# Performance work log

Hardware: AMD Instinct MI355X
Metric: run time of the kernel (lower is better)

## Reference

```python
import jax, jax.numpy as jnp
import numpy as np

B, T = 128, 512
V, P, K = 10002, 500, 20
DC, DP, DT = 300, 100, 50
D = DC + DP + DT
H = 256


def setup_inputs() -> dict:
    key = jax.random.key(0)
    ks = jax.random.split(key, 21)
    s = lambda i, shape: jax.random.normal(ks[i], shape, jnp.float32) * 0.05
    return dict(
        x=jax.random.randint(ks[0], (B, T), 0, V),
        y=jax.random.randint(ks[1], (B, T), 0, K),
        pre_tags=jax.random.randint(ks[2], (B, T), 0, K),
        pinyin_tags=jax.random.randint(ks[3], (B, T), 0, P),
        mask=jnp.ones((B, T), bool),
        char_emb=s(4, (V, DC)),
        tag_emb=s(5, (K, DT)),
        pinyin_emb=s(6, (P, DP)),
        w_ih_f=s(7, (4 * H, D)), w_hh_f=s(8, (4 * H, H)), b_ih_f=s(9, (4 * H,)), b_hh_f=s(10, (4 * H,)),
        w_ih_b=s(11, (4 * H, D)), w_hh_b=s(12, (4 * H, H)), b_ih_b=s(13, (4 * H,)), b_hh_b=s(14, (4 * H,)),
        w_out=s(15, (K, 2 * H)), b_out=s(16, (K,)),
        start_trans=s(17, (K,)), end_trans=s(18, (K,)), trans=s(19, (K, K)),
    )


def _lstm_dir(xs, w_ih, w_hh, b_ih, b_hh, reverse):
    # xs: [T,B,D]; precompute input projection for all steps (one big GEMM)
    pre = jnp.einsum('tbd,gd->tbg', xs, w_ih) + b_ih + b_hh  # [T,B,4H]
    bsz = xs.shape[1]

    def step(carry, gx):
        h, c = carry
        g = gx + h @ w_hh.T
        i, f, gg, o = jnp.split(g, 4, axis=-1)  # torch gate order i,f,g,o
        c = jax.nn.sigmoid(f) * c + jax.nn.sigmoid(i) * jnp.tanh(gg)
        h = jax.nn.sigmoid(o) * jnp.tanh(c)
        return (h, c), h

    init = (jnp.zeros((bsz, H), xs.dtype), jnp.zeros((bsz, H), xs.dtype))
    _, hs = jax.lax.scan(step, init, pre, reverse=reverse)
    return hs  # [T,B,H]


def _emissions(x, pre_tags, pinyin_tags, char_emb, tag_emb, pinyin_emb,
               w_ih_f, w_hh_f, b_ih_f, b_hh_f, w_ih_b, w_hh_b, b_ih_b, b_hh_b,
               w_out, b_out):
    emb = jnp.concatenate([char_emb[x], pinyin_emb[pinyin_tags], tag_emb[pre_tags]], axis=2)  # [B,T,D]
    xs = emb.transpose(1, 0, 2)  # [T,B,D]
    hf = _lstm_dir(xs, w_ih_f, w_hh_f, b_ih_f, b_hh_f, reverse=False)
    hb = _lstm_dir(xs, w_ih_b, w_hh_b, b_ih_b, b_hh_b, reverse=True)
    h = jnp.concatenate([hf, hb], axis=-1)  # [T,B,2H]
    return jnp.einsum('tbh,kh->tbk', h, w_out) + b_out  # emissions [T,B,K]


def _crf_nll(em, tags, mask, start, trans, end):
    # em [T,B,K] (time-major), torchcrf forward with reduction='sum'
    tg = tags.T  # [T,B]
    mk = mask.T.astype(em.dtype)  # [T,B]
    # gold-path score
    first = start[tg[0]] + jnp.take_along_axis(em[0], tg[0][:, None], 1)[:, 0]

    def num_step(score, inputs):
        e_t, t_prev, t_cur, m = inputs
        s = trans[t_prev, t_cur] + jnp.take_along_axis(e_t, t_cur[:, None], 1)[:, 0]
        return score + s * m, None

    score, _ = jax.lax.scan(num_step, first, (em[1:], tg[:-1], tg[1:], mk[1:]))
    last_idx = (mask.sum(1) - 1).astype(jnp.int32)
    last_tag = jnp.take_along_axis(tags, last_idx[:, None].astype(tags.dtype), 1)[:, 0]
    score = score + end[last_tag]
    # partition function via forward algorithm
    alpha0 = start[None, :] + em[0]  # [B,K]

    def den_step(alpha, inputs):
        e_t, m = inputs
        nxt = jax.nn.logsumexp(alpha[:, :, None] + trans[None, :, :] + e_t[:, None, :], axis=1)
        return jnp.where(m[:, None] > 0, nxt, alpha), None

    alpha, _ = jax.lax.scan(den_step, alpha0, (em[1:], mk[1:]))
    logZ = jax.nn.logsumexp(alpha + end[None, :], axis=1)
    llh = jnp.sum(score - logZ)
    return -llh  # module returns -crf(...)


def reference(x, y, pre_tags, pinyin_tags, mask, char_emb, tag_emb, pinyin_emb,
              w_ih_f, w_hh_f, b_ih_f, b_hh_f, w_ih_b, w_hh_b, b_ih_b, b_hh_b,
              w_out, b_out, start_trans, end_trans, trans):
    em = _emissions(x, pre_tags, pinyin_tags, char_emb, tag_emb, pinyin_emb,
                    w_ih_f, w_hh_f, b_ih_f, b_hh_f, w_ih_b, w_hh_b, b_ih_b, b_hh_b,
                    w_out, b_out)
    return _crf_nll(em, y, mask, start_trans, trans, end_trans)
```

## Files before the change

kernel.cpp:

```cpp
#include <hip/hip_runtime.h>
#include <hip/hip_bf16.h>

typedef __attribute__((ext_vector_type(8))) short short8;
typedef __attribute__((ext_vector_type(4))) float float4v;
typedef __attribute__((ext_vector_type(4))) int int4v;

__device__ __forceinline__ float sigmoidf_(float x) {
  return __fdividef(1.f, 1.f + __expf(-x));
}
__device__ __forceinline__ float tanhf_(float x) {
  float e = __expf(2.f * x);
  return 1.f - __fdividef(2.f, e + 1.f);
}
__device__ __forceinline__ float bflo(unsigned int v) {
  return __uint_as_float(v << 16);
}
__device__ __forceinline__ float bfhi(unsigned int v) {
  return __uint_as_float(v & 0xffff0000u);
}
__device__ __forceinline__ void barrier_lgkm() {
  asm volatile("s_waitcnt lgkmcnt(0)\n\ts_barrier" ::: "memory");
}

__device__ __forceinline__ unsigned int pack4_(float4 v, float inv) {
  int b0 = (int)rintf(v.x * inv), b1 = (int)rintf(v.y * inv);
  int b2 = (int)rintf(v.z * inv), b3 = (int)rintf(v.w * inv);
  return (unsigned int)((b0 & 0xff) | ((b1 & 0xff) << 8) | ((b2 & 0xff) << 16) |
                        ((b3 & 0xff) << 24));
}

__device__ __forceinline__ int sel4_(int4v v, int rr) {
  int a = (rr & 1) ? v[1] : v[0];
  int b = (rr & 1) ? v[3] : v[2];
  return (rr & 2) ? b : a;
}

__global__ __launch_bounds__(256) void wquant_kernel(
    const float* __restrict__ whh_f, const float* __restrict__ whh_b,
    unsigned int* __restrict__ wq, float* __restrict__ wsc) {
  const int wave_g = blockIdx.x * 4 + (threadIdx.x >> 6);
  const int lane = threadIdx.x & 63;
  const int dir = wave_g >> 10, row = wave_g & 1023;
  const float* __restrict__ src = (dir ? whh_b : whh_f) + (size_t)row * 256;
  float4 v = ((const float4*)src)[lane];
  float mx = fmaxf(fmaxf(fabsf(v.x), fabsf(v.y)), fmaxf(fabsf(v.z), fabsf(v.w)));
#pragma unroll
  for (int k = 32; k >= 1; k >>= 1) mx = fmaxf(mx, __shfl_xor(mx, k, 64));
  float inv = (mx > 0.f) ? __fdividef(127.f, mx) : 0.f;
  wq[(size_t)wave_g * 64 + lane] = pack4_(v, inv);
  if (lane == 0) wsc[wave_g] = (mx > 0.f) ? (mx / (127.f * 127.f)) : 0.f;
}

__global__ __launch_bounds__(256) void proj_gemm(
    const float* __restrict__ A, int rowsA, int Kdim, int col_off,
    const float* __restrict__ wf, const float* __restrict__ wb,
    const float* __restrict__ bf1, const float* __restrict__ bf2,
    const float* __restrict__ bb1, const float* __restrict__ bb2,
    __hip_bfloat16* __restrict__ out, int add_bias) {
  __shared__ __align__(16) __hip_bfloat16 As[128][40];
  __shared__ __align__(16) __hip_bfloat16 Bs[256][40];
  const int tid = threadIdx.x;
  const int m0 = blockIdx.x * 128, n0 = blockIdx.y * 256;
  const int lane = tid & 63, wave = tid >> 6;
  const int quad = lane >> 4, lm = lane & 15;
  float4v acc[2][16] = {};
  const int ksteps = (Kdim + 31) >> 5;
  const int r2 = tid >> 1, cbase = (tid & 1) << 4;
  const int rb = tid >> 4, cb = (tid & 15) * 2;
  for (int ks = 0; ks < ksteps; ++ks) {
    const int k0 = ks << 5;
#pragma unroll
    for (int e2 = 0; e2 < 8; ++e2) {
      int kk = k0 + cbase + 2 * e2;
      float b0 = 0.f, b1 = 0.f;
      if (m0 + r2 < rowsA && kk < Kdim) {
        float2 v = *(const float2*)(A + (size_t)(m0 + r2) * Kdim + kk);
        b0 = v.x;
        b1 = v.y;
      }
      As[r2][cbase + 2 * e2] = __float2bfloat16(b0);
      As[r2][cbase + 2 * e2 + 1] = __float2bfloat16(b1);
    }
#pragma unroll
    for (int j = 0; j < 16; ++j) {
      int n = n0 + rb + 16 * j;
      const float* __restrict__ wrow =
          (n < 1024) ? (wf + n * 450 + col_off) : (wb + (n - 1024) * 450 + col_off);
      int kk = k0 + cb;
      float b0 = 0.f, b1 = 0.f;
      if (kk < Kdim) {
        float2 v = *(const float2*)(wrow + kk);
        b0 = v.x;
        b1 = v.y;
      }
      Bs[rb + 16 * j][cb] = __float2bfloat16(b0);
      Bs[rb + 16 * j][cb + 1] = __float2bfloat16(b1);
    }
    __syncthreads();
    short8 af0 = *(const short8*)(&As[wave * 32 + lm][quad * 8]);
    short8 af1 = *(const short8*)(&As[wave * 32 + 16 + lm][quad * 8]);
#pragma unroll
    for (int t = 0; t < 16; ++t) {
      short8 bf = *(const short8*)(&Bs[t * 16 + lm][quad * 8]);
      acc[0][t] = __builtin_amdgcn_mfma_f32_16x16x32_bf16(af0, bf, acc[0][t], 0, 0, 0);
      acc[1][t] = __builtin_amdgcn_mfma_f32_16x16x32_bf16(af1, bf, acc[1][t], 0, 0, 0);
    }
    __syncthreads();
  }
#pragma unroll
  for (int mg = 0; mg < 2; ++mg) {
#pragma unroll
    for (int t = 0; t < 16; ++t) {
#pragma unroll
      for (int rr = 0; rr < 4; ++rr) {
        int m = m0 + wave * 32 + mg * 16 + quad * 4 + rr;
        int col = n0 + t * 16 + lm;
        if (m < rowsA) {
          float v = acc[mg][t][rr];
          if (add_bias)
            v += (col < 1024) ? (bf1[col] + bf2[col]) : (bb1[col - 1024] + bb2[col - 1024]);
          int dir = col >> 10, rq = col & 1023;
          int gate = rq >> 8, u = rq & 255;
          out[m * 2048 + dir * 1024 + u * 4 + gate] = __float2bfloat16(v);
        }
      }
    }
  }
}

__global__ __launch_bounds__(512, 2) void lstm_kernel(
    const unsigned int* __restrict__ wq, const float* __restrict__ wsc,
    const int* __restrict__ x, const int* __restrict__ ptags, const int* __restrict__ gtags,
    const char* __restrict__ char_proj, const char* __restrict__ pin_proj,
    const char* __restrict__ tag_proj, __hip_bfloat16* __restrict__ h_out) {
  extern __shared__ __align__(16) char smem[];
  __hip_bfloat16* hist = (__hip_bfloat16*)smem;
  char* hqb = smem + 16384;

  const int tid = threadIdx.x;
  const int w = tid >> 6, lane = tid & 63;
  const int quad = lane >> 4, lm = lane & 15;
  const int sel = lm >> 1;
  const int mt = sel >> 2, rr = sel & 3;
  const int unit = w * 32 + mt * 16 + quad * 4 + rr;
  const int chain = blockIdx.x;
  const int dir = chain >> 7;
  const int b = chain & 127;
  const int boff = b * 512;

  if (tid < 34) ((uint4*)hqb)[tid] = make_uint4(0, 0, 0, 0);

  const unsigned int* __restrict__ wqd = wq + (size_t)dir * 65536;
  int4v Wf[4][2][4];
#pragma unroll
  for (int g = 0; g < 4; ++g)
#pragma unroll
    for (int m = 0; m < 2; ++m) {
      const int row = g * 256 + w * 32 + m * 16 + lm;
#pragma unroll
      for (int kt = 0; kt < 4; ++kt)
        Wf[g][m][kt] = *(const int4v*)(wqd + row * 64 + kt * 16 + quad * 4);
    }
  float sc4[4];
#pragma unroll
  for (int g = 0; g < 4; ++g) sc4[g] = wsc[dir * 1024 + g * 256 + unit];
  __syncthreads();

  const int pre_off = dir * 2048 + unit * 8;
  float cst = 0.f;

  int t_cur = dir ? 511 : 0;
  int t_nxt = dir ? 510 : 1;
  int xc = x[boff + t_cur], pc_i = ptags[boff + t_cur], gc_i = gtags[boff + t_cur];
  uint2 vc = *(const uint2*)(char_proj + (size_t)xc * 4096 + pre_off);
  uint2 vp = *(const uint2*)(pin_proj + (size_t)pc_i * 4096 + pre_off);
  uint2 vg = *(const uint2*)(tag_proj + (size_t)gc_i * 4096 + pre_off);
  int xn = x[boff + t_nxt], pn = ptags[boff + t_nxt], gn = gtags[boff + t_nxt];

  for (int s = 0; s < 512; ++s) {
    const int cur = s & 1, nxt = cur ^ 1;
    const uint2 cv = vc, pv = vp, gv = vg;
    const int t_fut = dir ? (t_nxt > 0 ? t_nxt - 1 : 0) : (t_nxt < 511 ? t_nxt + 1 : 511);
    vc = *(const uint2*)(char_proj + (size_t)xn * 4096 + pre_off);
    vp = *(const uint2*)(pin_proj + (size_t)pn * 4096 + pre_off);
    vg = *(const uint2*)(tag_proj + (size_t)gn * 4096 + pre_off);
    xn = x[boff + t_fut];
    pn = ptags[boff + t_fut];
    gn = gtags[boff + t_fut];

    int4v acc[4][2] = {};
    const char* hqc = hqb + cur * 272;
#pragma unroll
    for (int kt = 0; kt < 4; ++kt) {
      int4v Bv = *(const int4v*)(hqc + kt * 64 + quad * 16);
#pragma unroll
      for (int g = 0; g < 4; ++g)
#pragma unroll
        for (int m = 0; m < 2; ++m)
          acc[g][m] = __builtin_amdgcn_mfma_i32_16x16x64_i8(Wf[g][m][kt], Bv, acc[g][m], 0, 0, 0);
    }

    int ai = mt ? sel4_(acc[0][1], rr) : sel4_(acc[0][0], rr);
    int af = mt ? sel4_(acc[1][1], rr) : sel4_(acc[1][0], rr);
    int ag = mt ? sel4_(acc[2][1], rr) : sel4_(acc[2][0], rr);
    int ao = mt ? sel4_(acc[3][1], rr) : sel4_(acc[3][0], rr);
    float gi = bflo(cv.x) + bflo(pv.x) + bflo(gv.x) + (float)ai * sc4[0];
    float gf = bfhi(cv.x) + bfhi(pv.x) + bfhi(gv.x) + (float)af * sc4[1];
    float gg = bflo(cv.y) + bflo(pv.y) + bflo(gv.y) + (float)ag * sc4[2];
    float go = bfhi(cv.y) + bfhi(pv.y) + bfhi(gv.y) + (float)ao * sc4[3];
    cst = sigmoidf_(gf) * cst + sigmoidf_(gi) * tanhf_(gg);
    float hval = sigmoidf_(go) * tanhf_(cst);
    if (!(lm & 1)) {
      ((signed char*)hqb)[nxt * 272 + unit] = (signed char)(int)rintf(hval * 127.f);
      hist[(s & 31) * 256 + unit] = __float2bfloat16(hval);
    }
    barrier_lgkm();
    if ((s & 15) == 15) {
      const int slotBase = (s & 31) & ~15;
      const int sBase = s - 15;
      const int row = tid >> 5;
      const int col16 = tid & 31;
      uint4 v = *(const uint4*)((const char*)hist + (slotBase + row) * 512 + col16 * 16);
      int step_r = sBase + row;
      int t_r = dir ? (511 - step_r) : step_r;
      *(uint4*)((char*)h_out + ((size_t)(chain * 512 + t_r) * 256) * 2 + col16 * 16) = v;
    }
    t_cur = t_nxt;
    t_nxt = t_fut;
  }
}

__global__ __launch_bounds__(256) void emis_kernel(
    const __hip_bfloat16* __restrict__ h_glob, const float* __restrict__ w_out,
    const float* __restrict__ b_out, float* __restrict__ em) {
  __shared__ __align__(16) __hip_bfloat16 As[64][40];
  __shared__ __align__(16) __hip_bfloat16 Bs[32][40];
  const int tid = threadIdx.x;
  const int n0 = blockIdx.x * 64;
  const int lane = tid & 63, wave = tid >> 6, quad = lane >> 4, lm = lane & 15;
  float4v acc[2] = {};
  const int r = tid >> 2, c0 = (tid & 3) << 3;
  const int rb = tid >> 3, cb = (tid & 7) << 2;
  for (int ks = 0; ks < 16; ++ks) {
    const int j0 = ks * 32;
    const int dirk = j0 >> 8, jin = j0 & 255;
    const int n = n0 + r, bb = n >> 9, tt = n & 511;
    const uint4* src =
        (const uint4*)(h_glob + ((size_t)(dirk * 128 + bb) * 512 + tt) * 256 + jin + c0);
    *(uint4*)(&As[r][c0]) = *src;
#pragma unroll
    for (int e = 0; e < 4; ++e) {
      float v = (rb < 20) ? w_out[rb * 512 + j0 + cb + e] : 0.f;
      Bs[rb][cb + e] = __float2bfloat16(v);
    }
    __syncthreads();
    short8 af = *(const short8*)(&As[wave * 16 + lm][quad * 8]);
#pragma unroll
    for (int t2 = 0; t2 < 2; ++t2) {
      short8 bf = *(const short8*)(&Bs[t2 * 16 + lm][quad * 8]);
      acc[t2] = __builtin_amdgcn_mfma_f32_16x16x32_bf16(af, bf, acc[t2], 0, 0, 0);
    }
    __syncthreads();
  }
#pragma unroll
  for (int t2 = 0; t2 < 2; ++t2) {
#pragma unroll
    for (int rr = 0; rr < 4; ++rr) {
      int col = t2 * 16 + lm;
      if (col < 20) {
        int n = n0 + wave * 16 + quad * 4 + rr;
        em[(size_t)n * 20 + col] = acc[t2][rr] + b_out[col];
      }
    }
  }
}

__global__ __launch_bounds__(64) void crf_kernel(
    const float* __restrict__ em, const int* __restrict__ y,
    const float* __restrict__ start_trans, const float* __restrict__ end_trans,
    const float* __restrict__ trans, float* __restrict__ partials) {
  const int b = blockIdx.x;
  const int lane = threadIdx.x;
  const int jj = lane < 20 ? lane : 19;
  const bool act = lane < 20;
  const float* __restrict__ emb = em + (size_t)b * 512 * 20;
  const int* __restrict__ yb = y + b * 512;

  float s_part = 0.f;
#pragma unroll
  for (int i = 0; i < 8; ++i) {
    int t = lane + 64 * i;
    int yc = yb[t];
    float v = emb[t * 20 + yc];
    v += (t == 0) ? start_trans[yc] : trans[yb[t - 1] * 20 + yc];
    s_part += v;
  }
#pragma unroll
  for (int k = 32; k >= 1; k >>= 1) s_part += __shfl_xor(s_part, k, 64);
  float score = s_part + end_trans[yb[511]];

  float ET[20];
#pragma unroll
  for (int i = 0; i < 20; ++i) ET[i] = __expf(trans[i * 20 + jj]);
  float alpha = act ? (start_trans[jj] + emb[jj]) : -1e30f;
  float P = alpha;
#pragma unroll
  for (int k = 32; k >= 1; k >>= 1) P = fmaxf(P, __shfl_xor(P, k, 64));

  float eC = emb[1 * 20 + jj];
  float eN = emb[2 * 20 + jj];
  for (int t = 1; t < 512; ++t) {
    if ((t & 15) == 0) {
      P = alpha;
#pragma unroll
      for (int k = 32; k >= 1; k >>= 1) P = fmaxf(P, __shfl_xor(P, k, 64));
    }
    float ex = __expf(alpha - P);
    float s0 = 0.f, s1 = 0.f;
#pragma unroll
    for (int i = 0; i < 20; i += 2) {
      float e0 = __int_as_float(__builtin_amdgcn_readlane(__float_as_int(ex), i));
      float e1 = __int_as_float(__builtin_amdgcn_readlane(__float_as_int(ex), i + 1));
      s0 = fmaf(e0, ET[i], s0);
      s1 = fmaf(e1, ET[i + 1], s1);
    }
    int tf = t + 2 < 512 ? t + 2 : 511;
    float eF = emb[tf * 20 + jj];
    if (act) alpha = P + __logf(s0 + s1) + eC;
    eC = eN;
    eN = eF;
  }
  float v = act ? (alpha + end_trans[jj]) : -1e30f;
  float Pz = v;
#pragma unroll
  for (int k = 32; k >= 1; k >>= 1) Pz = fmaxf(Pz, __shfl_xor(Pz, k, 64));
  float e2 = __expf(v - Pz);
#pragma unroll
  for (int k = 32; k >= 1; k >>= 1) e2 += __shfl_xor(e2, k, 64);
  float logZ = Pz + __logf(e2);
  if (lane == 0) partials[b] = logZ - score;
}

__global__ __launch_bounds__(128) void reduce_kernel(const float* __restrict__ partials,
                                                     float* __restrict__ out) {
  const int tid = threadIdx.x;
  float v = partials[tid];
#pragma unroll
  for (int k = 32; k >= 1; k >>= 1) v += __shfl_xor(v, k, 64);
  __shared__ float tmp[2];
  if ((tid & 63) == 0) tmp[tid >> 6] = v;
  __syncthreads();
  if (tid == 0) out[0] = tmp[0] + tmp[1];
}

extern "C" void kernel_launch(void* const* d_in, const int* in_sizes, int n_in,
                              void* d_out, int out_size, void* d_ws, size_t ws_size,
                              hipStream_t stream) {
  const int* x = (const int*)d_in[0];
  const int* y = (const int*)d_in[1];
  const int* pre_tags = (const int*)d_in[2];
  const int* pinyin_tags = (const int*)d_in[3];
  const float* char_emb = (const float*)d_in[5];
  const float* tag_emb = (const float*)d_in[6];
  const float* pinyin_emb = (const float*)d_in[7];
  const float* w_ih_f = (const float*)d_in[8];
  const float* w_hh_f = (const float*)d_in[9];
  const float* b_ih_f = (const float*)d_in[10];
  const float* b_hh_f = (const float*)d_in[11];
  const float* w_ih_b = (const float*)d_in[12];
  const float* w_hh_b = (const float*)d_in[13];
  const float* b_ih_b = (const float*)d_in[14];
  const float* b_hh_b = (const float*)d_in[15];
  const float* w_out = (const float*)d_in[16];
  const float* b_out = (const float*)d_in[17];
  const float* start_trans = (const float*)d_in[18];
  const float* end_trans = (const float*)d_in[19];
  const float* trans = (const float*)d_in[20];

  char* ws = (char*)d_ws;
  __hip_bfloat16* char_proj = (__hip_bfloat16*)(ws);
  __hip_bfloat16* pin_proj = (__hip_bfloat16*)(ws + 40968192);
  __hip_bfloat16* tag_proj = (__hip_bfloat16*)(ws + 43016192);
  __hip_bfloat16* h_glob = (__hip_bfloat16*)(ws + 43098112);
  float* em = (float*)(ws + 110206976);
  float* partials = (float*)(ws + 115449856);
  unsigned int* wq = (unsigned int*)(ws + 110206976);
  float* wsc = (float*)(ws + 110206976 + 524288);

  wquant_kernel<<<512, 256, 0, stream>>>(w_hh_f, w_hh_b, wq, wsc);

  proj_gemm<<<dim3(79, 8), 256, 0, stream>>>(char_emb, 10002, 300, 0, w_ih_f, w_ih_b,
                                             nullptr, nullptr, nullptr, nullptr, char_proj, 0);
  proj_gemm<<<dim3(4, 8), 256, 0, stream>>>(pinyin_emb, 500, 100, 300, w_ih_f, w_ih_b,
                                            nullptr, nullptr, nullptr, nullptr, pin_proj, 0);
  proj_gemm<<<dim3(1, 8), 256, 0, stream>>>(tag_emb, 20, 50, 400, w_ih_f, w_ih_b,
                                            b_ih_f, b_hh_f, b_ih_b, b_hh_b, tag_proj, 1);

  const int lstm_lds = 16928;
  hipFuncSetAttribute((const void*)lstm_kernel, hipFuncAttributeMaxDynamicSharedMemorySize,
                      lstm_lds);
  lstm_kernel<<<256, 512, lstm_lds, stream>>>(wq, wsc, x, pinyin_tags, pre_tags,
                                              (const char*)char_proj, (const char*)pin_proj,
                                              (const char*)tag_proj, h_glob);

  emis_kernel<<<1024, 256, 0, stream>>>(h_glob, w_out, b_out, em);
  crf_kernel<<<128, 64, 0, stream>>>(em, y, start_trans, end_trans, trans, partials);
  reduce_kernel<<<1, 128, 0, stream>>>(partials, (float*)d_out);
}
```

Baseline: 966.5 us.

## Precombine pinyin and tag projections into joint table; hoist h loads past barrier

Adds a kernel that precomputes the sum of the pinyin and tag input projections for all 500x20 combinations. This lets the LSTM recurrence gather two rows per step instead of three. The LSTM loop also loads the next step's quantized h operands right after the barrier, moves the bf16 history write after those loads, and adds an extra barrier before the periodic flush. The joint path only runs when the workspace is large enough, and it adds a 41MB table build plus an extra bf16 rounding of the summed projections.

After: 959.8 us. No clear change (-0.7%).

```diff
diff --git a/kernel.cpp b/kernel.cpp
--- a/kernel.cpp
+++ b/kernel.cpp
@@ -128,11 +128,32 @@
   }
 }
 
+__global__ __launch_bounds__(256) void pgsum_kernel(
+    const __hip_bfloat16* __restrict__ pin, const __hip_bfloat16* __restrict__ tag,
+    __hip_bfloat16* __restrict__ pg) {
+  const int r = blockIdx.x;
+  const int p = r / 20, g = r - p * 20;
+  const int i = threadIdx.x;
+  const short8 va = *(const short8*)(pin + (size_t)p * 2048 + i * 8);
+  const short8 vb = *(const short8*)(tag + (size_t)g * 2048 + i * 8);
+  short8 vo;
+#pragma unroll
+  for (int j = 0; j < 8; ++j) {
+    float a = __uint_as_float(((unsigned)(unsigned short)va[j]) << 16);
+    float b = __uint_as_float(((unsigned)(unsigned short)vb[j]) << 16);
+    __hip_bfloat16 o = __float2bfloat16(a + b);
+    vo[j] = *(short*)&o;
+  }
+  *(short8*)(pg + (size_t)r * 2048 + i * 8) = vo;
+}
+
+template <int USE_PG>
 __global__ __launch_bounds__(512, 2) void lstm_kernel(
     const unsigned int* __restrict__ wq, const float* __restrict__ wsc,
     const int* __restrict__ x, const int* __restrict__ ptags, const int* __restrict__ gtags,
     const char* __restrict__ char_proj, const char* __restrict__ pin_proj,
-    const char* __restrict__ tag_proj, __hip_bfloat16* __restrict__ h_out) {
+    const char* __restrict__ tag_proj, const char* __restrict__ pg_proj,
+    __hip_bfloat16* __restrict__ h_out) {
   extern __shared__ __align__(16) char smem[];
   __hip_bfloat16* hist = (__hip_bfloat16*)smem;
   char* hqb = smem + 16384;
@@ -171,51 +192,82 @@
 
   int t_cur = dir ? 511 : 0;
   int t_nxt = dir ? 510 : 1;
-  int xc = x[boff + t_cur], pc_i = ptags[boff + t_cur], gc_i = gtags[boff + t_cur];
-  uint2 vc = *(const uint2*)(char_proj + (size_t)xc * 4096 + pre_off);
-  uint2 vp = *(const uint2*)(pin_proj + (size_t)pc_i * 4096 + pre_off);
-  uint2 vg = *(const uint2*)(tag_proj + (size_t)gc_i * 4096 + pre_off);
-  int xn = x[boff + t_nxt], pn = ptags[boff + t_nxt], gn = gtags[boff + t_nxt];
+  uint2 vc, vp, vg;
+  int xn, pgn, pn, gn;
+  {
+    int xc = x[boff + t_cur], pc = ptags[boff + t_cur], gc = gtags[boff + t_cur];
+    vc = *(const uint2*)(char_proj + (size_t)xc * 4096 + pre_off);
+    if (USE_PG) {
+      vp = *(const uint2*)(pg_proj + (size_t)(pc * 20 + gc) * 4096 + pre_off);
+    } else {
+      vp = *(const uint2*)(pin_proj + (size_t)pc * 4096 + pre_off);
+      vg = *(const uint2*)(tag_proj + (size_t)gc * 4096 + pre_off);
+    }
+    xn = x[boff + t_nxt];
+    pn = ptags[boff + t_nxt];
+    gn = gtags[boff + t_nxt];
+    if (USE_PG) pgn = pn * 20 + gn;
+  }
+
+  int4v Bv[4];
+#pragma unroll
+  for (int kt = 0; kt < 4; ++kt)
+    Bv[kt] = *(const int4v*)(hqb + kt * 64 + quad * 16);
 
   for (int s = 0; s < 512; ++s) {
-    const int cur = s & 1, nxt = cur ^ 1;
+    const int nxt = (s & 1) ^ 1;
     const uint2 cv = vc, pv = vp, gv = vg;
     const int t_fut = dir ? (t_nxt > 0 ? t_nxt - 1 : 0) : (t_nxt < 511 ? t_nxt + 1 : 511);
     vc = *(const uint2*)(char_proj + (size_t)xn * 4096 + pre_off);
-    vp = *(const uint2*)(pin_proj + (size_t)pn * 4096 + pre_off);
-    vg = *(const uint2*)(tag_proj + (size_t)gn * 4096 + pre_off);
+    if (USE_PG) {
+      vp = *(const uint2*)(pg_proj + (size_t)pgn * 4096 + pre_off);
+    } else {
+      vp = *(const uint2*)(pin_proj + (size_t)pn * 4096 + pre_off);
+      vg = *(const uint2*)(tag_proj + (size_t)gn * 4096 + pre_off);
+    }
     xn = x[boff + t_fut];
     pn = ptags[boff + t_fut];
     gn = gtags[boff + t_fut];
+    if (USE_PG) pgn = pn * 20 + gn;
 
     int4v acc[4][2] = {};
-    const char* hqc = hqb + cur * 272;
 #pragma unroll
     for (int kt = 0; kt < 4; ++kt) {
-      int4v Bv = *(const int4v*)(hqc + kt * 64 + quad * 16);
 #pragma unroll
       for (int g = 0; g < 4; ++g)
 #pragma unroll
         for (int m = 0; m < 2; ++m)
-          acc[g][m] = __builtin_amdgcn_mfma_i32_16x16x64_i8(Wf[g][m][kt], Bv, acc[g][m], 0, 0, 0);
+          acc[g][m] = __builtin_amdgcn_mfma_i32_16x16x64_i8(Wf[g][m][kt], Bv[kt], acc[g][m], 0, 0, 0);
     }
 
     int ai = mt ? sel4_(acc[0][1], rr) : sel4_(acc[0][0], rr);
     int af = mt ? sel4_(acc[1][1], rr) : sel4_(acc[1][0], rr);
     int ag = mt ? sel4_(acc[2][1], rr) : sel4_(acc[2][0], rr);
     int ao = mt ? sel4_(acc[3][1], rr) : sel4_(acc[3][0], rr);
-    float gi = bflo(cv.x) + bflo(pv.x) + bflo(gv.x) + (float)ai * sc4[0];
-    float gf = bfhi(cv.x) + bfhi(pv.x) + bfhi(gv.x) + (float)af * sc4[1];
-    float gg = bflo(cv.y) + bflo(pv.y) + bflo(gv.y) + (float)ag * sc4[2];
-    float go = bfhi(cv.y) + bfhi(pv.y) + bfhi(gv.y) + (float)ao * sc4[3];
+    float gi, gf, gg, go;
+    if (USE_PG) {
+      gi = bflo(cv.x) + bflo(pv.x) + (float)ai * sc4[0];
+      gf = bfhi(cv.x) + bfhi(pv.x) + (float)af * sc4[1];
+      gg = bflo(cv.y) + bflo(pv.y) + (float)ag * sc4[2];
+      go = bfhi(cv.y) + bfhi(pv.y) + (float)ao * sc4[3];
+    } else {
+      gi = bflo(cv.x) + bflo(pv.x) + bflo(gv.x) + (float)ai * sc4[0];
+      gf = bfhi(cv.x) + bfhi(pv.x) + bfhi(gv.x) + (float)af * sc4[1];
+      gg = bflo(cv.y) + bflo(pv.y) + bflo(gv.y) + (float)ag * sc4[2];
+      go = bfhi(cv.y) + bfhi(pv.y) + bfhi(gv.y) + (float)ao * sc4[3];
+    }
     cst = sigmoidf_(gf) * cst + sigmoidf_(gi) * tanhf_(gg);
     float hval = sigmoidf_(go) * tanhf_(cst);
     if (!(lm & 1)) {
       ((signed char*)hqb)[nxt * 272 + unit] = (signed char)(int)rintf(hval * 127.f);
-      hist[(s & 31) * 256 + unit] = __float2bfloat16(hval);
     }
     barrier_lgkm();
+#pragma unroll
+    for (int kt = 0; kt < 4; ++kt)
+      Bv[kt] = *(const int4v*)(hqb + nxt * 272 + kt * 64 + quad * 16);
+    if (!(lm & 1)) hist[(s & 31) * 256 + unit] = __float2bfloat16(hval);
     if ((s & 15) == 15) {
+      barrier_lgkm();
       const int slotBase = (s & 31) & ~15;
       const int sBase = s - 15;
       const int row = tid >> 5;
@@ -386,6 +438,8 @@
   float* partials = (float*)(ws + 115449856);
   unsigned int* wq = (unsigned int*)(ws + 110206976);
   float* wsc = (float*)(ws + 110206976 + 524288);
+  __hip_bfloat16* pg_proj = (__hip_bfloat16*)(ws + 115450368);
+  const bool use_pg = ws_size >= (size_t)115450368 + 40960000;
 
   wquant_kernel<<<512, 256, 0, stream>>>(w_hh_f, w_hh_b, wq, wsc);
 
@@ -395,13 +449,24 @@
                                             nullptr, nullptr, nullptr, nullptr, pin_proj, 0);
   proj_gemm<<<dim3(1, 8), 256, 0, stream>>>(tag_emb, 20, 50, 400, w_ih_f, w_ih_b,
                                             b_ih_f, b_hh_f, b_ih_b, b_hh_b, tag_proj, 1);
+  if (use_pg) pgsum_kernel<<<10000, 256, 0, stream>>>(pin_proj, tag_proj, pg_proj);
 
   const int lstm_lds = 16928;
-  hipFuncSetAttribute((const void*)lstm_kernel, hipFuncAttributeMaxDynamicSharedMemorySize,
-                      lstm_lds);
-  lstm_kernel<<<256, 512, lstm_lds, stream>>>(wq, wsc, x, pinyin_tags, pre_tags,
-                                              (const char*)char_proj, (const char*)pin_proj,
-                                              (const char*)tag_proj, h_glob);
+  if (use_pg) {
+    hipFuncSetAttribute((const void*)lstm_kernel<1>, hipFuncAttributeMaxDynamicSharedMemorySize,
+                        lstm_lds);
+    lstm_kernel<1><<<256, 512, lstm_lds, stream>>>(wq, wsc, x, pinyin_tags, pre_tags,
+                                                   (const char*)char_proj, (const char*)pin_proj,
+                                                   (const char*)tag_proj, (const char*)pg_proj,
+                                                   h_glob);
+  } else {
+    hipFuncSetAttribute((const void*)lstm_kernel<0>, hipFuncAttributeMaxDynamicSharedMemorySize,
+                        lstm_lds);
+    lstm_kernel<0><<<256, 512, lstm_lds, stream>>>(wq, wsc, x, pinyin_tags, pre_tags,
+                                                   (const char*)char_proj, (const char*)pin_proj,
+                                                   (const char*)tag_proj, (const char*)pg_proj,
+                                                   h_glob);
+  }
 
   emis_kernel<<<1024, 256, 0, stream>>>(h_glob, w_out, b_out, em);
   crf_kernel<<<128, 64, 0, stream>>>(em, y, start_trans, end_trans, trans, partials);
```
